# Performance work log

Measured on AMD Instinct MI355X. Metric: run time of the kernel, lower is better.

## Reference

```python
import jax, jax.numpy as jnp
import numpy as np

B, N, C, K = 4, 4096, 512, 20
HID = C // 8  # dim // downrate
EPS = 1e-5
SLOPE = 0.2


def leaky_relu(x):
    return jnp.where(x >= 0, x, SLOPE * x)


def setup_inputs() -> dict:
    key = jax.random.key(0)
    k1, k2, k3, k4 = jax.random.split(key, 4)
    x_features = jax.random.normal(k1, (B, N, C), dtype=jnp.float32)
    xyz_coords = jax.random.normal(k2, (B, N, 3), dtype=jnp.float32)
    # conv1: Conv2d(2C -> HID, 1x1, bias=False) as dense matrix (HID, 2C)
    w1 = jax.random.normal(k3, (HID, 2 * C), dtype=jnp.float32) * (1.0 / np.sqrt(2 * C))
    g1 = jnp.ones((HID,), jnp.float32)
    b1 = jnp.zeros((HID,), jnp.float32)
    # conv2: Conv1d(HID -> C, 1, bias=False) as (C, HID)
    w2 = jax.random.normal(k4, (C, HID), dtype=jnp.float32) * (1.0 / np.sqrt(HID))
    g2 = jnp.ones((C,), jnp.float32)
    b2 = jnp.zeros((C,), jnp.float32)
    return {"x_features": x_features, "xyz_coords": xyz_coords,
            "w1": w1, "g1": g1, "b1": b1, "w2": w2, "g2": g2, "b2": b2}


def _knn_idx(xyz):
    # pairwise squared distance: ||a||^2 + ||b||^2 - 2 a.b  -> (B, N, N)
    sq = jnp.sum(xyz * xyz, -1)
    d = sq[:, :, None] + sq[:, None, :] - 2.0 * jnp.einsum('bnc,bmc->bnm', xyz, xyz)
    # topk smallest == topk largest of -d
    _, idx = jax.lax.top_k(-d, K)  # (B, N, K)
    return idx


def reference(x_features, xyz_coords, w1, g1, b1, w2, g2, b2):
    idx = _knn_idx(xyz_coords)  # (B,N,K) int32
    # gather neighbor features: (B,N,K,C)
    neigh = x_features[jnp.arange(B)[:, None, None], idx]
    query = x_features[:, :, None, :]  # (B,N,1,C)
    # fused = [neigh - query, query] along channels -> (B,N,K,2C)
    fused = jnp.concatenate([neigh - query, jnp.broadcast_to(query, neigh.shape)], axis=-1)
    # conv1 (1x1) -> (B,N,K,HID)
    h = jnp.einsum('bnkc,dc->bnkd', fused, w1)
    # BatchNorm2d over (B,N,K) per channel (training-mode batch stats, biased var)
    mu = jnp.mean(h, axis=(0, 1, 2))
    var = jnp.mean((h - mu) ** 2, axis=(0, 1, 2))
    h = leaky_relu(g1 * (h - mu) * jax.lax.rsqrt(var + EPS) + b1)
    # max over k neighbors -> (B,N,HID)
    h = jnp.max(h, axis=2)
    # conv2 (1x1) -> (B,N,C)
    y = jnp.einsum('bnd,ed->bne', h, w2)
    mu2 = jnp.mean(y, axis=(0, 1))
    var2 = jnp.mean((y - mu2) ** 2, axis=(0, 1))
    y = leaky_relu(g2 * (y - mu2) * jax.lax.rsqrt(var2 + EPS) + b2)
    return y  # (B, N, C), matches output_features.permute(0,2,1)
```

## Files before the change

### kernel.cpp

```cpp
#include <hip/hip_runtime.h>
#include <hip/hip_bf16.h>
#include <stdint.h>

#define NPTS 4096
#define NBATCH 4
#define NCH 512
#define NK 20
#define NHID 64
#define NROWS 16384
#define S1SH 32
#define S2SH 8

typedef __attribute__((ext_vector_type(8))) short bf16x8;
typedef __attribute__((ext_vector_type(4))) float f32x4;

__device__ __forceinline__ float bf2f(unsigned short u) {
    return __uint_as_float(((unsigned)u) << 16);
}
__device__ __forceinline__ unsigned short f2bf(float f) {
    unsigned u = __float_as_uint(f);
    unsigned r = 0x7FFFu + ((u >> 16) & 1u);
    return (unsigned short)((u + r) >> 16);
}
__device__ __forceinline__ float leaky(float x) { return x >= 0.f ? x : 0.2f * x; }
__device__ __forceinline__ int dtflag(const void* g) {
    return (((const unsigned short*)g)[0] == 0x3F80u) ? 0 : 1;
}

__device__ __forceinline__ void split8(const float* p, bf16x8& hi, bf16x8& lo) {
    float4 v0 = *(const float4*)p;
    float4 v1 = *(const float4*)(p + 4);
    float vv[8] = {v0.x, v0.y, v0.z, v0.w, v1.x, v1.y, v1.z, v1.w};
#pragma unroll
    for (int i = 0; i < 8; ++i) {
        unsigned u = __float_as_uint(vv[i]);
        hi[i] = (short)(u >> 16);
        float hf = __uint_as_float(u & 0xFFFF0000u);
        lo[i] = (short)f2bf(vv[i] - hf);
    }
}

template <int CTRL, int RM>
__device__ __forceinline__ float dppmin_f(float v) {
    int s = __builtin_amdgcn_update_dpp(__float_as_int(v), __float_as_int(v), CTRL, RM, 0xF, false);
    return fminf(v, __int_as_float(s));
}
template <int CTRL, int RM>
__device__ __forceinline__ unsigned dppmin_u(unsigned v) {
    unsigned s = (unsigned)__builtin_amdgcn_update_dpp((int)v, (int)v, CTRL, RM, 0xF, false);
    return v < s ? v : s;
}
__device__ __forceinline__ float wave_min_f63(float v) {
    v = dppmin_f<0x111, 0xF>(v);
    v = dppmin_f<0x112, 0xF>(v);
    v = dppmin_f<0x114, 0xF>(v);
    v = dppmin_f<0x118, 0xF>(v);
    v = dppmin_f<0x142, 0xA>(v);
    v = dppmin_f<0x143, 0xC>(v);
    return v;
}
__device__ __forceinline__ unsigned wave_min_u63(unsigned v) {
    v = dppmin_u<0x111, 0xF>(v);
    v = dppmin_u<0x112, 0xF>(v);
    v = dppmin_u<0x114, 0xF>(v);
    v = dppmin_u<0x118, 0xF>(v);
    v = dppmin_u<0x142, 0xA>(v);
    v = dppmin_u<0x143, 0xC>(v);
    return v;
}

__global__ __launch_bounds__(256) void k_wsplit(const float* __restrict__ w1f,
                                                const void* __restrict__ g1,
                                                unsigned short* __restrict__ Whi,
                                                unsigned short* __restrict__ Wlo,
                                                float* __restrict__ sumsz) {
    int t = threadIdx.x;
    {
        int i = blockIdx.x * 192 + t;
        if (t < 192) sumsz[i] = 0.f;
    }
    if (dtflag(g1) != 1) return;
    int id = blockIdx.x * 256 + t;
    int e0 = id * 4;
    int n = e0 >> 9, k = e0 & 511;
    const float* src = w1f + ((n < 64) ? (size_t)n * 1024 + k
                                       : (size_t)(n - 64) * 1024 + 512 + k);
    float4 v = *(const float4*)src;
    float vv[4] = {v.x, v.y, v.z, v.w};
    unsigned short hs[4], ls[4];
#pragma unroll
    for (int i = 0; i < 4; ++i) {
        unsigned u = __float_as_uint(vv[i]);
        hs[i] = (unsigned short)(u >> 16);
        float hf = __uint_as_float(u & 0xFFFF0000u);
        ls[i] = f2bf(vv[i] - hf);
    }
    *(ushort4*)(Whi + e0) = make_ushort4(hs[0], hs[1], hs[2], hs[3]);
    *(ushort4*)(Wlo + e0) = make_ushort4(ls[0], ls[1], ls[2], ls[3]);
}

__global__ __launch_bounds__(256) void k_pq(const void* __restrict__ xv,
                                            const unsigned short* __restrict__ w1u,
                                            const unsigned short* __restrict__ Whi,
                                            const unsigned short* __restrict__ Wlo,
                                            float* __restrict__ PQ,
                                            const void* __restrict__ g1) {
    int f = dtflag(g1);
    int t = threadIdx.x;
    int l = t & 63, w = t >> 6;
    int m0 = blockIdx.x * 16;
    int lr = l & 15, lk = (l >> 4) * 8;
    int n0a = w * 32, n0b = n0a + 16;
    f32x4 acc0 = {0.f, 0.f, 0.f, 0.f};
    f32x4 acc1 = {0.f, 0.f, 0.f, 0.f};
    if (!f) {
        const unsigned short* xp = (const unsigned short*)xv + (size_t)(m0 + lr) * 512 + lk;
        int na = n0a + lr, nb = n0b + lr;
        size_t wao = (na < 64) ? (size_t)na * 1024 : (size_t)(na - 64) * 1024 + 512;
        size_t wbo = (nb < 64) ? (size_t)nb * 1024 : (size_t)(nb - 64) * 1024 + 512;
        const unsigned short* wpa = w1u + wao + lk;
        const unsigned short* wpb = w1u + wbo + lk;
#pragma unroll 4
        for (int k0 = 0; k0 < 512; k0 += 32) {
            bf16x8 a  = *(const bf16x8*)(xp + k0);
            bf16x8 b0 = *(const bf16x8*)(wpa + k0);
            bf16x8 b1 = *(const bf16x8*)(wpb + k0);
            acc0 = __builtin_amdgcn_mfma_f32_16x16x32_bf16(a, b0, acc0, 0, 0, 0);
            acc1 = __builtin_amdgcn_mfma_f32_16x16x32_bf16(a, b1, acc1, 0, 0, 0);
        }
    } else {
        const float* xp = (const float*)xv + (size_t)(m0 + lr) * 512 + lk;
        const unsigned short* wha = Whi + (size_t)(n0a + lr) * 512 + lk;
        const unsigned short* wla = Wlo + (size_t)(n0a + lr) * 512 + lk;
        const unsigned short* whb = Whi + (size_t)(n0b + lr) * 512 + lk;
        const unsigned short* wlb = Wlo + (size_t)(n0b + lr) * 512 + lk;
        f32x4 hh0 = {0.f,0.f,0.f,0.f}, hl0 = {0.f,0.f,0.f,0.f}, lh0 = {0.f,0.f,0.f,0.f};
        f32x4 hh1 = {0.f,0.f,0.f,0.f}, hl1 = {0.f,0.f,0.f,0.f}, lh1 = {0.f,0.f,0.f,0.f};
#pragma unroll 4
        for (int k0 = 0; k0 < 512; k0 += 32) {
            bf16x8 ah, al;
            split8(xp + k0, ah, al);
            bf16x8 bh0 = *(const bf16x8*)(wha + k0);
            bf16x8 bl0 = *(const bf16x8*)(wla + k0);
            bf16x8 bh1 = *(const bf16x8*)(whb + k0);
            bf16x8 bl1 = *(const bf16x8*)(wlb + k0);
            hh0 = __builtin_amdgcn_mfma_f32_16x16x32_bf16(ah, bh0, hh0, 0, 0, 0);
            hh1 = __builtin_amdgcn_mfma_f32_16x16x32_bf16(ah, bh1, hh1, 0, 0, 0);
            hl0 = __builtin_amdgcn_mfma_f32_16x16x32_bf16(ah, bl0, hl0, 0, 0, 0);
            hl1 = __builtin_amdgcn_mfma_f32_16x16x32_bf16(ah, bl1, hl1, 0, 0, 0);
            lh0 = __builtin_amdgcn_mfma_f32_16x16x32_bf16(al, bh0, lh0, 0, 0, 0);
            lh1 = __builtin_amdgcn_mfma_f32_16x16x32_bf16(al, bh1, lh1, 0, 0, 0);
        }
#pragma unroll
        for (int r = 0; r < 4; ++r) {
            acc0[r] = hh0[r] + hl0[r] + lh0[r];
            acc1[r] = hh1[r] + hl1[r] + lh1[r];
        }
    }
    int cr = (l >> 4) * 4, cc = l & 15;
    float* o = PQ + (size_t)(m0 + cr) * 128;
#pragma unroll
    for (int r = 0; r < 4; ++r) {
        o[(size_t)r * 128 + n0a + cc] = acc0[r];
        o[(size_t)r * 128 + n0b + cc] = acc1[r];
    }
}

__global__ __launch_bounds__(512, 4) void k_knn(const void* __restrict__ xyzv,
                                                int* __restrict__ idxb,
                                                const void* __restrict__ g1) {
    __shared__ float4 sp[NPTS];
    const float FINF = __int_as_float(0x7F800000);
    int f = dtflag(g1);
    int t = threadIdx.x;
    int b = blockIdx.y;
    for (int p = t; p < NPTS; p += 512) {
        size_t base = ((size_t)b * NPTS + p) * 3;
        float fx, fy, fz;
        if (!f) {
            const unsigned short* xu = (const unsigned short*)xyzv;
            fx = bf2f(xu[base]); fy = bf2f(xu[base + 1]); fz = bf2f(xu[base + 2]);
        } else {
            const float* xf = (const float*)xyzv;
            fx = xf[base]; fy = xf[base + 1]; fz = xf[base + 2];
        }
        float sq = __fadd_rn(__fadd_rn(__fmul_rn(fx, fx), __fmul_rn(fy, fy)), __fmul_rn(fz, fz));
        sp[p] = make_float4(fx, fy, fz, sq);
    }
    __syncthreads();
    int lane = t & 63, wave = t >> 6;
    int nl = blockIdx.x * 8 + wave;
    float4 q = sp[nl];
    float qx = q.x, qy = q.y, qz = q.z, sqn = q.w;
    float D[64];
    float gv[8]; int gj[8];
#pragma unroll
    for (int g = 0; g < 8; ++g) { gv[g] = FINF; gj[g] = 0; }
#pragma unroll
    for (int j = 0; j < 64; ++j) {
        float4 p = sp[j * 64 + lane];
        float dot = __fadd_rn(__fadd_rn(__fmul_rn(qx, p.x), __fmul_rn(qy, p.y)),
                              __fmul_rn(qz, p.z));
        float d = __fsub_rn(__fadd_rn(sqn, p.w), __fmul_rn(2.0f, dot));
        D[j] = d;
        int g = j >> 3;
        bool lt = d < gv[g];
        gv[g] = lt ? d : gv[g];
        gj[g] = lt ? j : gj[g];
    }
    int myout = 0;
    for (int k = 0; k < NK; ++k) {
        float bv = gv[0]; int bj = gj[0];
#pragma unroll
        for (int g = 1; g < 8; ++g) {
            bool lt = gv[g] < bv;
            bv = lt ? gv[g] : bv;
            bj = lt ? gj[g] : bj;
        }
        float red = wave_min_f63(bv);
        float s_mv = __int_as_float(__builtin_amdgcn_readlane(__float_as_int(red), 63));
        unsigned long long tied = __ballot(bv == s_mv);
        int sL, sj;
        if (__popcll(tied) == 1) {
            sL = (int)__builtin_ctzll(tied);
            sj = __builtin_amdgcn_readlane(bj, sL);
        } else {
            unsigned bjm = (bv == s_mv) ? (unsigned)bj : 0xFFFFFFFFu;
            unsigned rj = wave_min_u63(bjm);
            sj = __builtin_amdgcn_readlane((int)rj, 63);
            unsigned long long t2 = __ballot((bv == s_mv) && (bj == sj));
            sL = (int)__builtin_ctzll(t2);
        }
        int sm = (sj << 6) | sL;
        if (lane == k) myout = sm;
        bool iwin = (lane == sL);
#pragma unroll
        for (int gg = 0; gg < 8; ++gg) {
            if (gg == (sj >> 3)) {
#pragma unroll
                for (int jj = 0; jj < 8; ++jj) {
                    int j = gg * 8 + jj;
                    bool rem = iwin && (j == sj);
                    D[j] = rem ? FINF : D[j];
                }
                float nv = D[gg * 8]; int nj = gg * 8;
#pragma unroll
                for (int u = 1; u < 8; ++u) {
                    bool lt = D[gg * 8 + u] < nv;
                    nv = lt ? D[gg * 8 + u] : nv;
                    nj = lt ? gg * 8 + u : nj;
                }
                if (iwin) { gv[gg] = nv; gj[gg] = nj; }
            }
        }
    }
    if (lane < NK)
        idxb[((size_t)b * NPTS + nl) * NK + lane] = myout;
}

__global__ __launch_bounds__(256) void k_gather(const float* __restrict__ PQ,
                                                const int* __restrict__ idxb,
                                                float* __restrict__ Hmax,
                                                float* __restrict__ Hmin,
                                                float* __restrict__ sums1) {
    __shared__ float bs[64], bq[64];
    int t = threadIdx.x;
    if (t < 64) { bs[t] = 0.f; bq[t] = 0.f; }
    __syncthreads();
    int lane = t & 63, wave = t >> 6;
    int rowbase = blockIdx.x * 16 + wave * 4;
    int b = blockIdx.x >> 8;
    size_t boff = (size_t)b * NPTS;
    float lsum = 0.f, lsq = 0.f;
    for (int r = 0; r < 4; ++r) {
        int row = rowbase + r;
        float q = PQ[(size_t)row * 128 + 64 + lane] - PQ[(size_t)row * 128 + lane];
        const int* ip = idxb + (size_t)row * NK;
        int idx[20];
        *(int4*)&idx[0]  = *(const int4*)(ip + 0);
        *(int4*)&idx[4]  = *(const int4*)(ip + 4);
        *(int4*)&idx[8]  = *(const int4*)(ip + 8);
        *(int4*)&idx[12] = *(const int4*)(ip + 12);
        *(int4*)&idx[16] = *(const int4*)(ip + 16);
        float hmax = -3.4e38f, hmin = 3.4e38f;
#pragma unroll
        for (int k = 0; k < NK; ++k) {
            int m = idx[k] & (NPTS - 1);
            float p = PQ[(boff + m) * 128 + lane];
            float h = p + q;
            lsum += h; lsq += h * h;
            hmax = fmaxf(hmax, h); hmin = fminf(hmin, h);
        }
        Hmax[(size_t)row * 64 + lane] = hmax;
        Hmin[(size_t)row * 64 + lane] = hmin;
    }
    atomicAdd(&bs[lane], lsum);
    atomicAdd(&bq[lane], lsq);
    __syncthreads();
    float* sh = sums1 + (blockIdx.x & (S1SH - 1)) * 128;
    if (t < 64) { atomicAdd(&sh[t], bs[t]); atomicAdd(&sh[64 + t], bq[t]); }
}

__global__ __launch_bounds__(256) void k_gemm2(const float* __restrict__ Hmax,
                                               const float* __restrict__ Hmin,
                                               const float* __restrict__ sums1,
                                               const void* __restrict__ g1,
                                               const void* __restrict__ b1,
                                               const void* __restrict__ w2,
                                               void* __restrict__ out,
                                               float* __restrict__ sums2) {
    int f = dtflag(g1);
    __shared__ float hs[32][68];
    __shared__ float wl[128][68];
    __shared__ float s2[512], q2[512];
    __shared__ float a1s[64], c1s[64];
    int t = threadIdx.x;
    int rowbase = blockIdx.x * 32;
    s2[t] = 0.f; s2[t + 256] = 0.f; q2[t] = 0.f; q2[t + 256] = 0.f;
    if (t < 64) {
        float ssum = 0.f, ssq = 0.f;
#pragma unroll 4
        for (int s = 0; s < S1SH; ++s) {
            ssum += sums1[s * 128 + t];
            ssq  += sums1[s * 128 + 64 + t];
        }
        const float inv = 1.0f / 327680.0f;
        float mu = ssum * inv;
        float var = fmaxf(ssq * inv - mu * mu, 0.f);
        float rstd = rsqrtf(var + 1e-5f);
        float gvv = f ? ((const float*)g1)[t] : bf2f(((const unsigned short*)g1)[t]);
        float bvv = f ? ((const float*)b1)[t] : bf2f(((const unsigned short*)b1)[t]);
        float a = gvv * rstd;
        a1s[t] = a;
        c1s[t] = bvv - mu * a;
    }
    __syncthreads();
    {
        int rl = t >> 3, dqs = (t & 7) * 8;
#pragma unroll
        for (int i = 0; i < 2; ++i) {
            int d0 = dqs + i * 4;
            float4 M4 = *(const float4*)&Hmax[(size_t)(rowbase + rl) * 64 + d0];
            float4 m4 = *(const float4*)&Hmin[(size_t)(rowbase + rl) * 64 + d0];
            float4 A = *(const float4*)&a1s[d0];
            float4 C = *(const float4*)&c1s[d0];
            float4 o;
            o.x = leaky(A.x * (A.x >= 0.f ? M4.x : m4.x) + C.x);
            o.y = leaky(A.y * (A.y >= 0.f ? M4.y : m4.y) + C.y);
            o.z = leaky(A.z * (A.z >= 0.f ? M4.z : m4.z) + C.z);
            o.w = leaky(A.w * (A.w >= 0.f ? M4.w : m4.w) + C.w);
            *(float4*)&hs[rl][d0] = o;
        }
    }
    int tx = t & 15, ty = t >> 4;
    int wel = t >> 2, wdq = (t & 3) * 16;
#pragma unroll 1
    for (int eb = 0; eb < 512; eb += 128) {
        __syncthreads();
        {
#pragma unroll
            for (int i = 0; i < 4; ++i) {
                int d0 = wdq + i * 4;
                size_t offA = (size_t)(eb + wel) * 64 + d0;
                size_t offB = (size_t)(eb + wel + 64) * 64 + d0;
                float4 oA, oB;
                if (!f) {
                    ushort4 wA = *(const ushort4*)((const unsigned short*)w2 + offA);
                    ushort4 wB = *(const ushort4*)((const unsigned short*)w2 + offB);
                    oA = make_float4(bf2f(wA.x), bf2f(wA.y), bf2f(wA.z), bf2f(wA.w));
                    oB = make_float4(bf2f(wB.x), bf2f(wB.y), bf2f(wB.z), bf2f(wB.w));
                } else {
                    oA = *(const float4*)((const float*)w2 + offA);
                    oB = *(const float4*)((const float*)w2 + offB);
                }
                *(float4*)&wl[wel][d0] = oA;
                *(float4*)&wl[wel + 64][d0] = oB;
            }
        }
        __syncthreads();
        float acc[2][8] = {};
#pragma unroll 2
        for (int dq = 0; dq < 16; ++dq) {
            float4 hx[2], wx[8];
#pragma unroll
            for (int i = 0; i < 2; ++i) hx[i] = *(const float4*)&hs[ty * 2 + i][dq * 4];
#pragma unroll
            for (int j = 0; j < 8; ++j) wx[j] = *(const float4*)&wl[tx + 16 * j][dq * 4];
#pragma unroll
            for (int i = 0; i < 2; ++i)
#pragma unroll
                for (int j = 0; j < 8; ++j) {
                    acc[i][j] = fmaf(hx[i].x, wx[j].x, acc[i][j]);
                    acc[i][j] = fmaf(hx[i].y, wx[j].y, acc[i][j]);
                    acc[i][j] = fmaf(hx[i].z, wx[j].z, acc[i][j]);
                    acc[i][j] = fmaf(hx[i].w, wx[j].w, acc[i][j]);
                }
        }
        float se[8] = {}, sqe[8] = {};
#pragma unroll
        for (int i = 0; i < 2; ++i)
#pragma unroll
            for (int j = 0; j < 8; ++j) {
                float y = acc[i][j];
                se[j] += y; sqe[j] += y * y;
                size_t oi = (size_t)(rowbase + ty * 2 + i) * 512 + eb + tx + 16 * j;
                if (!f) ((unsigned short*)out)[oi] = f2bf(y);
                else    ((float*)out)[oi] = y;
            }
#pragma unroll
        for (int j = 0; j < 8; ++j) {
            se[j] += __shfl_xor(se[j], 16, 64);
            se[j] += __shfl_xor(se[j], 32, 64);
            sqe[j] += __shfl_xor(sqe[j], 16, 64);
            sqe[j] += __shfl_xor(sqe[j], 32, 64);
        }
        if (((t & 63) >> 4) == 0) {
#pragma unroll
            for (int j = 0; j < 8; ++j) {
                atomicAdd(&s2[eb + tx + 16 * j], se[j]);
                atomicAdd(&q2[eb + tx + 16 * j], sqe[j]);
            }
        }
    }
    __syncthreads();
    float* s2g = sums2 + (blockIdx.x & (S2SH - 1)) * 1024;
    atomicAdd(&s2g[t], s2[t]);
    atomicAdd(&s2g[t + 256], s2[t + 256]);
    atomicAdd(&s2g[512 + t], q2[t]);
    atomicAdd(&s2g[512 + t + 256], q2[t + 256]);
}

__global__ void k_stats2(const float* __restrict__ sums2,
                         const void* __restrict__ g2,
                         const void* __restrict__ b2,
                         float* __restrict__ a2c2) {
    int f = dtflag(g2);
    int t = threadIdx.x;
    float ssum = 0.f, ssq = 0.f;
#pragma unroll
    for (int s = 0; s < S2SH; ++s) {
        ssum += sums2[s * 1024 + t];
        ssq  += sums2[s * 1024 + 512 + t];
    }
    const float inv = 1.0f / 16384.0f;
    float mu = ssum * inv;
    float var = fmaxf(ssq * inv - mu * mu, 0.f);
    float rstd = rsqrtf(var + 1e-5f);
    float gvv = f ? ((const float*)g2)[t] : bf2f(((const unsigned short*)g2)[t]);
    float bvv = f ? ((const float*)b2)[t] : bf2f(((const unsigned short*)b2)[t]);
    float a = gvv * rstd;
    a2c2[t] = a;
    a2c2[512 + t] = bvv - mu * a;
}

__global__ __launch_bounds__(256) void k_final(void* __restrict__ out,
                                               const float* __restrict__ a2c2,
                                               const void* __restrict__ g2) {
    int f = dtflag(g2);
    size_t base = ((size_t)blockIdx.x * 256 + threadIdx.x) * 8;
    int e0 = (int)(base & 511);
    float a[8], c[8];
    *(float4*)&a[0] = *(const float4*)&a2c2[e0];
    *(float4*)&a[4] = *(const float4*)&a2c2[e0 + 4];
    *(float4*)&c[0] = *(const float4*)&a2c2[512 + e0];
    *(float4*)&c[4] = *(const float4*)&a2c2[512 + e0 + 4];
    if (!f) {
        unsigned short* po = (unsigned short*)out + base;
        uint4 v = *(const uint4*)po;
        unsigned w[4] = {v.x, v.y, v.z, v.w};
        unsigned r[4];
#pragma unroll
        for (int i = 0; i < 4; ++i) {
            float f0 = __uint_as_float(w[i] << 16);
            float f1 = __uint_as_float(w[i] & 0xFFFF0000u);
            float y0 = leaky(a[2 * i] * f0 + c[2 * i]);
            float y1 = leaky(a[2 * i + 1] * f1 + c[2 * i + 1]);
            r[i] = (unsigned)f2bf(y0) | ((unsigned)f2bf(y1) << 16);
        }
        *(uint4*)po = make_uint4(r[0], r[1], r[2], r[3]);
    } else {
        float* po = (float*)out + base;
        float4 v0 = *(const float4*)po;
        float4 v1 = *(const float4*)(po + 4);
        float v[8] = {v0.x, v0.y, v0.z, v0.w, v1.x, v1.y, v1.z, v1.w};
#pragma unroll
        for (int i = 0; i < 8; ++i) v[i] = leaky(a[i] * v[i] + c[i]);
        *(float4*)po = make_float4(v[0], v[1], v[2], v[3]);
        *(float4*)(po + 4) = make_float4(v[4], v[5], v[6], v[7]);
    }
}

extern "C" void kernel_launch(void* const* d_in, const int* in_sizes, int n_in,
                              void* d_out, int out_size, void* d_ws, size_t ws_size,
                              hipStream_t stream) {
    const void* x   = d_in[0];
    const void* xyz = d_in[1];
    const void* w1  = d_in[2];
    const void* g1  = d_in[3];
    const void* b1  = d_in[4];
    const void* w2  = d_in[5];
    const void* g2  = d_in[6];
    const void* b2  = d_in[7];

    float* ws    = (float*)d_ws;
    float* PQ    = ws;
    float* Hmax  = ws + 2097152;
    float* Hmin  = ws + 3145728;
    float* sums1 = ws + 4194304;
    float* sums2 = ws + 4198400;
    float* a2c2  = ws + 4206592;
    int*   idxb  = (int*)(ws + 4207616);
    unsigned short* Whi = (unsigned short*)(ws + 4535296);
    unsigned short* Wlo = (unsigned short*)(ws + 4568064);

    k_wsplit<<<64, 256, 0, stream>>>((const float*)w1, g1, Whi, Wlo, sums1);
    k_pq<<<1024, 256, 0, stream>>>(x, (const unsigned short*)w1, Whi, Wlo, PQ, g1);
    k_knn<<<dim3(512, 4), 512, 0, stream>>>(xyz, idxb, g1);
    k_gather<<<1024, 256, 0, stream>>>(PQ, idxb, Hmax, Hmin, sums1);
    k_gemm2<<<512, 256, 0, stream>>>(Hmax, Hmin, sums1, g1, b1, w2, d_out, sums2);
    k_stats2<<<1, 512, 0, stream>>>(sums2, g2, b2, a2c2);
    k_final<<<4096, 256, 0, stream>>>(d_out, a2c2, g2);
}
```

Measured before the change: 267.1 us.

## Move conv2 GEMM to bf16 MFMA with hi/lo split-precision emulation

```diff
diff --git a/kernel.cpp b/kernel.cpp
--- a/kernel.cpp
+++ b/kernel.cpp
@@ -9,7 +9,7 @@
 #define NHID 64
 #define NROWS 16384
 #define S1SH 32
-#define S2SH 8
+#define S2SH 16
 
 typedef __attribute__((ext_vector_type(8))) short bf16x8;
 typedef __attribute__((ext_vector_type(4))) float f32x4;
@@ -70,33 +70,51 @@
 }
 
 __global__ __launch_bounds__(256) void k_wsplit(const float* __restrict__ w1f,
+                                                const float* __restrict__ w2f,
                                                 const void* __restrict__ g1,
                                                 unsigned short* __restrict__ Whi,
                                                 unsigned short* __restrict__ Wlo,
+                                                unsigned short* __restrict__ Wh2,
+                                                unsigned short* __restrict__ Wl2,
                                                 float* __restrict__ sumsz) {
     int t = threadIdx.x;
+    int id = blockIdx.x * 256 + t;
+    sumsz[id] = 0.f;
+    if (id < 20480 - 16384) sumsz[id + 16384] = 0.f;
+    if (dtflag(g1) != 1) return;
     {
-        int i = blockIdx.x * 192 + t;
-        if (t < 192) sumsz[i] = 0.f;
-    }
-    if (dtflag(g1) != 1) return;
-    int id = blockIdx.x * 256 + t;
-    int e0 = id * 4;
-    int n = e0 >> 9, k = e0 & 511;
-    const float* src = w1f + ((n < 64) ? (size_t)n * 1024 + k
-                                       : (size_t)(n - 64) * 1024 + 512 + k);
-    float4 v = *(const float4*)src;
-    float vv[4] = {v.x, v.y, v.z, v.w};
-    unsigned short hs[4], ls[4];
-#pragma unroll
-    for (int i = 0; i < 4; ++i) {
-        unsigned u = __float_as_uint(vv[i]);
-        hs[i] = (unsigned short)(u >> 16);
-        float hf = __uint_as_float(u & 0xFFFF0000u);
-        ls[i] = f2bf(vv[i] - hf);
-    }
-    *(ushort4*)(Whi + e0) = make_ushort4(hs[0], hs[1], hs[2], hs[3]);
-    *(ushort4*)(Wlo + e0) = make_ushort4(ls[0], ls[1], ls[2], ls[3]);
+        int e0 = id * 4;
+        int n = e0 >> 9, k = e0 & 511;
+        const float* src = w1f + ((n < 64) ? (size_t)n * 1024 + k
+                                           : (size_t)(n - 64) * 1024 + 512 + k);
+        float4 v = *(const float4*)src;
+        float vv[4] = {v.x, v.y, v.z, v.w};
+        unsigned short hs[4], ls[4];
+#pragma unroll
+        for (int i = 0; i < 4; ++i) {
+            unsigned u = __float_as_uint(vv[i]);
+            hs[i] = (unsigned short)(u >> 16);
+            float hf = __uint_as_float(u & 0xFFFF0000u);
+            ls[i] = f2bf(vv[i] - hf);
+        }
+        *(ushort4*)(Whi + e0) = make_ushort4(hs[0], hs[1], hs[2], hs[3]);
+        *(ushort4*)(Wlo + e0) = make_ushort4(ls[0], ls[1], ls[2], ls[3]);
+    }
+    {
+        int e0 = id * 2;
+        float2 v = *(const float2*)(w2f + e0);
+        float vv[2] = {v.x, v.y};
+        unsigned short hs[2], ls[2];
+#pragma unroll
+        for (int i = 0; i < 2; ++i) {
+            unsigned u = __float_as_uint(vv[i]);
+            hs[i] = (unsigned short)(u >> 16);
+            float hf = __uint_as_float(u & 0xFFFF0000u);
+            ls[i] = f2bf(vv[i] - hf);
+        }
+        *(ushort2*)(Wh2 + e0) = make_ushort2(hs[0], hs[1]);
+        *(ushort2*)(Wl2 + e0) = make_ushort2(ls[0], ls[1]);
+    }
 }
 
 __global__ __launch_bounds__(256) void k_pq(const void* __restrict__ xv,
@@ -306,16 +324,15 @@
                                                const float* __restrict__ sums1,
                                                const void* __restrict__ g1,
                                                const void* __restrict__ b1,
-                                               const void* __restrict__ w2,
+                                               const unsigned short* __restrict__ Wh2,
+                                               const unsigned short* __restrict__ Wl2,
+                                               const void* __restrict__ w2raw,
                                                void* __restrict__ out,
                                                float* __restrict__ sums2) {
     int f = dtflag(g1);
-    __shared__ float hs[32][68];
-    __shared__ float wl[128][68];
+    __shared__ float a1s[64], c1s[64];
     __shared__ float s2[512], q2[512];
-    __shared__ float a1s[64], c1s[64];
     int t = threadIdx.x;
-    int rowbase = blockIdx.x * 32;
     s2[t] = 0.f; s2[t + 256] = 0.f; q2[t] = 0.f; q2[t + 256] = 0.f;
     if (t < 64) {
         float ssum = 0.f, ssq = 0.f;
@@ -335,91 +352,68 @@
         c1s[t] = bvv - mu * a;
     }
     __syncthreads();
-    {
-        int rl = t >> 3, dqs = (t & 7) * 8;
-#pragma unroll
-        for (int i = 0; i < 2; ++i) {
-            int d0 = dqs + i * 4;
-            float4 M4 = *(const float4*)&Hmax[(size_t)(rowbase + rl) * 64 + d0];
-            float4 m4 = *(const float4*)&Hmin[(size_t)(rowbase + rl) * 64 + d0];
-            float4 A = *(const float4*)&a1s[d0];
-            float4 C = *(const float4*)&c1s[d0];
-            float4 o;
-            o.x = leaky(A.x * (A.x >= 0.f ? M4.x : m4.x) + C.x);
-            o.y = leaky(A.y * (A.y >= 0.f ? M4.y : m4.y) + C.y);
-            o.z = leaky(A.z * (A.z >= 0.f ? M4.z : m4.z) + C.z);
-            o.w = leaky(A.w * (A.w >= 0.f ? M4.w : m4.w) + C.w);
-            *(float4*)&hs[rl][d0] = o;
-        }
-    }
-    int tx = t & 15, ty = t >> 4;
-    int wel = t >> 2, wdq = (t & 3) * 16;
-#pragma unroll 1
-    for (int eb = 0; eb < 512; eb += 128) {
-        __syncthreads();
-        {
-#pragma unroll
-            for (int i = 0; i < 4; ++i) {
-                int d0 = wdq + i * 4;
-                size_t offA = (size_t)(eb + wel) * 64 + d0;
-                size_t offB = (size_t)(eb + wel + 64) * 64 + d0;
-                float4 oA, oB;
-                if (!f) {
-                    ushort4 wA = *(const ushort4*)((const unsigned short*)w2 + offA);
-                    ushort4 wB = *(const ushort4*)((const unsigned short*)w2 + offB);
-                    oA = make_float4(bf2f(wA.x), bf2f(wA.y), bf2f(wA.z), bf2f(wA.w));
-                    oB = make_float4(bf2f(wB.x), bf2f(wB.y), bf2f(wB.z), bf2f(wB.w));
-                } else {
-                    oA = *(const float4*)((const float*)w2 + offA);
-                    oB = *(const float4*)((const float*)w2 + offB);
-                }
-                *(float4*)&wl[wel][d0] = oA;
-                *(float4*)&wl[wel + 64][d0] = oB;
-            }
-        }
-        __syncthreads();
-        float acc[2][8] = {};
+    int lane = t & 63, w = t >> 6;
+    int lr = lane & 15, lk = (lane >> 4) * 8;
+    int rowo = blockIdx.x * 16;
+    int row = rowo + lr;
+    bf16x8 ah[2], al[2];
+#pragma unroll
+    for (int c = 0; c < 2; ++c) {
+        int off = c * 32 + lk;
+        const float* Mx = Hmax + (size_t)row * 64 + off;
+        const float* Mn = Hmin + (size_t)row * 64 + off;
+        float4 M0 = *(const float4*)Mx, M1 = *(const float4*)(Mx + 4);
+        float4 m0 = *(const float4*)Mn, m1 = *(const float4*)(Mn + 4);
+        float Ms[8] = {M0.x, M0.y, M0.z, M0.w, M1.x, M1.y, M1.z, M1.w};
+        float ms[8] = {m0.x, m0.y, m0.z, m0.w, m1.x, m1.y, m1.z, m1.w};
+#pragma unroll
+        for (int e = 0; e < 8; ++e) {
+            float A = a1s[off + e], C = c1s[off + e];
+            float h = leaky(A * (A >= 0.f ? Ms[e] : ms[e]) + C);
+            unsigned u = __float_as_uint(h);
+            ah[c][e] = (short)(u >> 16);
+            al[c][e] = (short)f2bf(h - __uint_as_float(u & 0xFFFF0000u));
+        }
+    }
+    int cr = (lane >> 4) * 4, cc = lane & 15;
 #pragma unroll 2
-        for (int dq = 0; dq < 16; ++dq) {
-            float4 hx[2], wx[8];
-#pragma unroll
-            for (int i = 0; i < 2; ++i) hx[i] = *(const float4*)&hs[ty * 2 + i][dq * 4];
-#pragma unroll
-            for (int j = 0; j < 8; ++j) wx[j] = *(const float4*)&wl[tx + 16 * j][dq * 4];
-#pragma unroll
-            for (int i = 0; i < 2; ++i)
-#pragma unroll
-                for (int j = 0; j < 8; ++j) {
-                    acc[i][j] = fmaf(hx[i].x, wx[j].x, acc[i][j]);
-                    acc[i][j] = fmaf(hx[i].y, wx[j].y, acc[i][j]);
-                    acc[i][j] = fmaf(hx[i].z, wx[j].z, acc[i][j]);
-                    acc[i][j] = fmaf(hx[i].w, wx[j].w, acc[i][j]);
-                }
-        }
-        float se[8] = {}, sqe[8] = {};
-#pragma unroll
-        for (int i = 0; i < 2; ++i)
-#pragma unroll
-            for (int j = 0; j < 8; ++j) {
-                float y = acc[i][j];
-                se[j] += y; sqe[j] += y * y;
-                size_t oi = (size_t)(rowbase + ty * 2 + i) * 512 + eb + tx + 16 * j;
-                if (!f) ((unsigned short*)out)[oi] = f2bf(y);
-                else    ((float*)out)[oi] = y;
-            }
-#pragma unroll
-        for (int j = 0; j < 8; ++j) {
-            se[j] += __shfl_xor(se[j], 16, 64);
-            se[j] += __shfl_xor(se[j], 32, 64);
-            sqe[j] += __shfl_xor(sqe[j], 16, 64);
-            sqe[j] += __shfl_xor(sqe[j], 32, 64);
-        }
-        if (((t & 63) >> 4) == 0) {
-#pragma unroll
-            for (int j = 0; j < 8; ++j) {
-                atomicAdd(&s2[eb + tx + 16 * j], se[j]);
-                atomicAdd(&q2[eb + tx + 16 * j], sqe[j]);
-            }
+    for (int j = 0; j < 8; ++j) {
+        int n0 = w * 128 + j * 16;
+        f32x4 hh = {0.f,0.f,0.f,0.f}, hl = {0.f,0.f,0.f,0.f}, lh = {0.f,0.f,0.f,0.f};
+        if (!f) {
+            const unsigned short* wb = (const unsigned short*)w2raw + (size_t)(n0 + lr) * 64;
+            bf16x8 b0 = *(const bf16x8*)(wb + lk);
+            bf16x8 b1 = *(const bf16x8*)(wb + 32 + lk);
+            hh = __builtin_amdgcn_mfma_f32_16x16x32_bf16(ah[0], b0, hh, 0, 0, 0);
+            lh = __builtin_amdgcn_mfma_f32_16x16x32_bf16(al[0], b0, lh, 0, 0, 0);
+            hh = __builtin_amdgcn_mfma_f32_16x16x32_bf16(ah[1], b1, hh, 0, 0, 0);
+            lh = __builtin_amdgcn_mfma_f32_16x16x32_bf16(al[1], b1, lh, 0, 0, 0);
+        } else {
+            const unsigned short* bh = Wh2 + (size_t)(n0 + lr) * 64;
+            const unsigned short* bl = Wl2 + (size_t)(n0 + lr) * 64;
+            bf16x8 bh0 = *(const bf16x8*)(bh + lk), bl0 = *(const bf16x8*)(bl + lk);
+            bf16x8 bh1 = *(const bf16x8*)(bh + 32 + lk), bl1 = *(const bf16x8*)(bl + 32 + lk);
+            hh = __builtin_amdgcn_mfma_f32_16x16x32_bf16(ah[0], bh0, hh, 0, 0, 0);
+            hl = __builtin_amdgcn_mfma_f32_16x16x32_bf16(ah[0], bl0, hl, 0, 0, 0);
+            lh = __builtin_amdgcn_mfma_f32_16x16x32_bf16(al[0], bh0, lh, 0, 0, 0);
+            hh = __builtin_amdgcn_mfma_f32_16x16x32_bf16(ah[1], bh1, hh, 0, 0, 0);
+            hl = __builtin_amdgcn_mfma_f32_16x16x32_bf16(ah[1], bl1, hl, 0, 0, 0);
+            lh = __builtin_amdgcn_mfma_f32_16x16x32_bf16(al[1], bh1, lh, 0, 0, 0);
+        }
+        float se = 0.f, sqe = 0.f;
+#pragma unroll
+        for (int r = 0; r < 4; ++r) {
+            float y = hh[r] + hl[r] + lh[r];
+            se += y; sqe += y * y;
+            size_t oi = (size_t)(rowo + cr + r) * 512 + n0 + cc;
+            if (!f) ((unsigned short*)out)[oi] = f2bf(y);
+            else    ((float*)out)[oi] = y;
+        }
+        se += __shfl_xor(se, 16, 64);  se += __shfl_xor(se, 32, 64);
+        sqe += __shfl_xor(sqe, 16, 64); sqe += __shfl_xor(sqe, 32, 64);
+        if ((lane >> 4) == 0) {
+            atomicAdd(&s2[n0 + cc], se);
+            atomicAdd(&q2[n0 + cc], sqe);
         }
     }
     __syncthreads();
@@ -508,16 +502,20 @@
     float* Hmin  = ws + 3145728;
     float* sums1 = ws + 4194304;
     float* sums2 = ws + 4198400;
-    float* a2c2  = ws + 4206592;
-    int*   idxb  = (int*)(ws + 4207616);
-    unsigned short* Whi = (unsigned short*)(ws + 4535296);
-    unsigned short* Wlo = (unsigned short*)(ws + 4568064);
-
-    k_wsplit<<<64, 256, 0, stream>>>((const float*)w1, g1, Whi, Wlo, sums1);
+    float* a2c2  = ws + 4214784;
+    int*   idxb  = (int*)(ws + 4215808);
+    unsigned short* Whi = (unsigned short*)(ws + 4543488);
+    unsigned short* Wlo = (unsigned short*)(ws + 4576256);
+    unsigned short* Wh2 = (unsigned short*)(ws + 4609024);
+    unsigned short* Wl2 = (unsigned short*)(ws + 4625408);
+
+    k_wsplit<<<64, 256, 0, stream>>>((const float*)w1, (const float*)w2, g1,
+                                     Whi, Wlo, Wh2, Wl2, sums1);
     k_pq<<<1024, 256, 0, stream>>>(x, (const unsigned short*)w1, Whi, Wlo, PQ, g1);
     k_knn<<<dim3(512, 4), 512, 0, stream>>>(xyz, idxb, g1);
     k_gather<<<1024, 256, 0, stream>>>(PQ, idxb, Hmax, Hmin, sums1);
-    k_gemm2<<<512, 256, 0, stream>>>(Hmax, Hmin, sums1, g1, b1, w2, d_out, sums2);
+    k_gemm2<<<1024, 256, 0, stream>>>(Hmax, Hmin, sums1, g1, b1,
+                                      Wh2, Wl2, w2, d_out, sums2);
     k_stats2<<<1, 512, 0, stream>>>(sums2, g2, b2, a2c2);
     k_final<<<4096, 256, 0, stream>>>(d_out, a2c2, g2);
 }
```

Result: faster. 255.3 us (-4.4%).
